# Optimization experiments

Measured on AMD Instinct MI355X. Metric: run time of the kernel, lower is better.

## Reference

```python
import jax, jax.numpy as jnp
import numpy as np

N = 50000      # nodes
E = 800000     # edges (before self-loops)
F_IN = 128     # input features
HID = 64       # hidden width
CLS = 40       # classes
NEG_SLOPE = 0.2  # PyG GATConv default
EPS = 1e-16


def setup_inputs() -> dict:
    key = jax.random.key(0)
    ks = jax.random.split(key, 16)

    def lin(k, fi, fo):
        return jax.random.normal(k, (fi, fo), jnp.float32) / np.float32(np.sqrt(fi))

    def att(k, f):
        return jax.random.normal(k, (f,), jnp.float32) / np.float32(np.sqrt(f))

    return {
        "x": jax.random.normal(ks[0], (N, F_IN), jnp.float32),
        "edge_index": jax.random.randint(ks[1], (2, E), 0, N, dtype=jnp.int64),
        "W1": lin(ks[2], F_IN, HID), "a_src1": att(ks[3], HID), "a_dst1": att(ks[4], HID), "b1": jnp.zeros((HID,), jnp.float32),
        "W2": lin(ks[5], HID, HID),  "a_src2": att(ks[6], HID), "a_dst2": att(ks[7], HID), "b2": jnp.zeros((HID,), jnp.float32),
        "W3": lin(ks[8], HID, CLS),  "a_src3": att(ks[9], CLS), "a_dst3": att(ks[10], CLS), "b3": jnp.zeros((CLS,), jnp.float32),
    }


def gat_layer(x, src, dst, W, a_src, a_dst, b, n):
    # Single-head GATConv (PyG semantics, heads=1, add_self_loops already applied).
    h = x @ W                                  # [n, out]
    s_src = h @ a_src                          # [n]
    s_dst = h @ a_dst                          # [n]
    e = jax.nn.leaky_relu(s_src[src] + s_dst[dst], NEG_SLOPE)  # [E']
    # softmax over incoming edges of each destination node
    m = jax.ops.segment_max(e, dst, num_segments=n)            # [n]
    e = jnp.exp(e - m[dst])
    denom = jax.ops.segment_sum(e, dst, num_segments=n)        # [n]
    alpha = e / (denom[dst] + EPS)                             # [E']
    out = jax.ops.segment_sum(h[src] * alpha[:, None], dst, num_segments=n)
    return out + b


def reference(x, edge_index, W1, a_src1, a_dst1, b1, W2, a_src2, a_dst2, b2, W3, a_src3, a_dst3, b3):
    n = x.shape[0]
    loop = jnp.arange(n, dtype=edge_index.dtype)
    src = jnp.concatenate([edge_index[0], loop])   # add self-loops (GATConv default)
    dst = jnp.concatenate([edge_index[1], loop])

    h = gat_layer(x, src, dst, W1, a_src1, a_dst1, b1, n)
    h = jax.nn.gelu(h, approximate=False)          # torch F.gelu default = exact erf
    h = gat_layer(h, src, dst, W2, a_src2, a_dst2, b2, n)
    h = jax.nn.gelu(h, approximate=False)
    out = gat_layer(h, src, dst, W3, a_src3, a_dst3, b3, n)
    return out
```

## Files before the change

kernel.cpp:

```cpp
#include <hip/hip_runtime.h>
#include <hip/hip_bf16.h>
#include <math.h>


#define PAD_CAP 64
#define SCAT_BLOCKS 128

__device__ __forceinline__ int detect64(const int* __restrict__ ei) {
  int any = 0;
#pragma unroll
  for (int i = 1; i < 64; i += 2) any |= ei[i];
  return any == 0;
}

__device__ __forceinline__ void load_edge(const int* __restrict__ ei, int E,
                                          int e, int is64, int n, int& s,
                                          int& d) {
  if (is64) {
    s = ei[2 * e];
    d = ei[2 * (E + e)];
  } else {
    s = ei[e];
    d = ei[E + e];
  }
  s = min(max(s, 0), n - 1);
  d = min(max(d, 0), n - 1);
}

template <int FROW>
__device__ __forceinline__ void gather8(const unsigned short* __restrict__ hu,
                                        int s0, float w0, int deg, int q,
                                        bool act, float& ax, float& ay,
                                        float& az, float& aw_) {
  int ss[8];
  float ww[8];
  uint2 hv[8];
#pragma unroll
  for (int j = 0; j < 8; ++j) {
    ss[j] = __shfl(s0, 4 * j + q);
    ww[j] = __shfl(w0, 4 * j + q);
  }
#pragma unroll
  for (int j = 0; j < 8; ++j) {
    hv[j].x = 0u;
    hv[j].y = 0u;
    if (act) hv[j] = *(const uint2*)(hu + (size_t)ss[j] * FROW);
  }
#pragma unroll
  for (int j = 0; j < 8; ++j) {
    ax = fmaf(ww[j], __uint_as_float(hv[j].x << 16), ax);
    ay = fmaf(ww[j], __uint_as_float(hv[j].x & 0xffff0000u), ay);
    az = fmaf(ww[j], __uint_as_float(hv[j].y << 16), az);
    aw_ = fmaf(ww[j], __uint_as_float(hv[j].y & 0xffff0000u), aw_);
  }
  const int dg4 = (deg + 3) >> 2;
  for (int g = 8; g < dg4; ++g) {
    const int ss1 = __shfl(s0, 4 * g + q);
    const float ww1 = __shfl(w0, 4 * g + q);
    uint2 hv1;
    hv1.x = 0u;
    hv1.y = 0u;
    if (act) hv1 = *(const uint2*)(hu + (size_t)ss1 * FROW);
    ax = fmaf(ww1, __uint_as_float(hv1.x << 16), ax);
    ay = fmaf(ww1, __uint_as_float(hv1.x & 0xffff0000u), ay);
    az = fmaf(ww1, __uint_as_float(hv1.y << 16), az);
    aw_ = fmaf(ww1, __uint_as_float(hv1.y & 0xffff0000u), aw_);
  }
}


template <int F_IN, int F_OUT, bool SCATTER>
__global__ __launch_bounds__(256) void gemm_att(
    const float* __restrict__ x, const float* __restrict__ W,
    const float* __restrict__ a_src, const float* __restrict__ a_dst,
    __hip_bfloat16* __restrict__ h, float* __restrict__ s_src,
    float* __restrict__ s_dst, int n, const int* __restrict__ ei, int E,
    int* __restrict__ deg, unsigned short* __restrict__ col) {
  if constexpr (SCATTER) {
    if (blockIdx.x < SCAT_BLOCKS) {
      const int is64 = detect64(ei);
      const int total = E + n;
      const int stride = SCAT_BLOCKS * 256;
      int e = blockIdx.x * 256 + threadIdx.x;
      while (e < total) {
        int sv[8], dv[8], va[8], pos[8];
#pragma unroll
        for (int j = 0; j < 8; ++j) {
          const int ee = e + j * stride;
          va[j] = (ee < total);
          int s = 0, d = 0;
          if (va[j]) {
            if (ee < E) load_edge(ei, E, ee, is64, n, s, d);
            else { s = ee - E; d = ee - E; }
          }
          sv[j] = s;
          dv[j] = d;
        }
#pragma unroll
        for (int j = 0; j < 8; ++j)
          pos[j] = va[j] ? atomicAdd(deg + dv[j], 1) : PAD_CAP;
#pragma unroll
        for (int j = 0; j < 8; ++j)
          if (va[j] && pos[j] < PAD_CAP)
            col[((size_t)dv[j] << 6) + pos[j]] = (unsigned short)sv[j];
        e += 8 * stride;
      }
      return;
    }
  }

  constexpr int TF = F_OUT / 4;
  __shared__ float Xt[F_IN * 65];
  __shared__ float red[2][4][64];
  const int wave = threadIdx.x >> 6, lane = threadIdx.x & 63;
  const int bid = SCATTER ? (int)blockIdx.x - SCAT_BLOCKS : (int)blockIdx.x;
  const int nb0 = bid * 64;
  const int node = nb0 + lane;

  {
    constexpr int Q = F_IN / 4;
    for (int i = threadIdx.x; i < 64 * Q; i += 256) {
      const int nd = i / Q, k4 = i % Q;
      float4 v = {0.f, 0.f, 0.f, 0.f};
      if (nb0 + nd < n)
        v = *(const float4*)(x + (size_t)(nb0 + nd) * F_IN + 4 * k4);
      Xt[(4 * k4 + 0) * 65 + nd] = v.x;
      Xt[(4 * k4 + 1) * 65 + nd] = v.y;
      Xt[(4 * k4 + 2) * 65 + nd] = v.z;
      Xt[(4 * k4 + 3) * 65 + nd] = v.w;
    }
  }
  __syncthreads();

  const int f0 = __builtin_amdgcn_readfirstlane(wave * TF);
  float acc[TF];
#pragma unroll
  for (int ff = 0; ff < TF; ++ff) acc[ff] = 0.f;

#pragma unroll 4
  for (int k = 0; k < F_IN; ++k) {
    const float xk = Xt[k * 65 + lane];
#pragma unroll
    for (int ff = 0; ff < TF; ++ff)
      acc[ff] = fmaf(xk, W[k * F_OUT + f0 + ff], acc[ff]);
  }

  float pa = 0.f, pb = 0.f;
#pragma unroll
  for (int ff = 0; ff < TF; ++ff) {
    pa = fmaf(acc[ff], a_src[f0 + ff], pa);
    pb = fmaf(acc[ff], a_dst[f0 + ff], pb);
  }
  if (node < n) {
#pragma unroll
    for (int ff = 0; ff < TF; ++ff)
      h[(size_t)node * F_OUT + f0 + ff] = __float2bfloat16(acc[ff]);
  }
  red[0][wave][lane] = pa;
  red[1][wave][lane] = pb;
  __syncthreads();
  if (wave == 0 && node < n) {
    s_src[node] = red[0][0][lane] + red[0][1][lane] + red[0][2][lane] +
                  red[0][3][lane];
    s_dst[node] = red[1][0][lane] + red[1][1][lane] + red[1][2][lane] +
                  red[1][3][lane];
  }
}

template <int F_OUT>
__global__ __launch_bounds__(1024, 4) void aggr_gemm(
    const unsigned short* __restrict__ col, const int* __restrict__ deg_arr,
    const float* __restrict__ ssrc, const float* __restrict__ sdst,
    const __hip_bfloat16* __restrict__ h_in, const float* __restrict__ bias_in,
    const float* __restrict__ W, const float* __restrict__ a_src,
    const float* __restrict__ a_dst, __hip_bfloat16* __restrict__ h_out,
    float* __restrict__ ssrc_out, float* __restrict__ sdst_out, int n) {
  constexpr int F_IN = 64;
  constexpr int NW = F_OUT / 4;
  __shared__ float Xt[F_IN * 65];
  __shared__ float red[2][16][64];
  const int wave = threadIdx.x >> 6, lane = threadIdx.x & 63;
  const int q = lane >> 4, t4 = lane & 15;
  const int nb0 = blockIdx.x * 64;

  float4 bv = make_float4(0.f, 0.f, 0.f, 0.f);
  if (lane < 16) bv = *(const float4*)(bias_in + 4 * lane);

  const unsigned short* __restrict__ hu = (const unsigned short*)h_in + 4 * t4;

  int degv[4], s0v[4];
  float sdv[4], svalv[4];
#pragma unroll
  for (int r = 0; r < 4; ++r) {
    const int d = nb0 + 4 * wave + r;
    const bool ok = d < n;
    degv[r] = ok ? min(deg_arr[d], PAD_CAP) : 0;
    sdv[r] = ok ? sdst[d] : 0.f;
    s0v[r] = 0;
    if (lane < degv[r]) s0v[r] = col[((size_t)d << 6) + lane];
  }
#pragma unroll
  for (int r = 0; r < 4; ++r) {
    svalv[r] = 0.f;
    if (lane < degv[r]) svalv[r] = ssrc[s0v[r]];
  }
  float w0v[4], invv[4];
#pragma unroll
  for (int r = 0; r < 4; ++r) {
    float w = 0.f;
    if (lane < degv[r]) {
      float t = svalv[r] + sdv[r];
      t = t > 0.f ? t : 0.2f * t;
      w = __expf(t);
    }
    w0v[r] = w;
  }
#pragma unroll
  for (int r = 0; r < 4; ++r) {
    float den = w0v[r];
#pragma unroll
    for (int off = 32; off > 0; off >>= 1) den += __shfl_xor(den, off);
    invv[r] = 1.f / (den + 1e-16f);
  }

  uint2 hv[4][8];
#pragma unroll
  for (int r = 0; r < 4; ++r) {
#pragma unroll
    for (int j = 0; j < 8; ++j) {
      const int ss = __shfl(s0v[r], 4 * j + q);
      hv[r][j] = *(const uint2*)(hu + (size_t)ss * F_IN);
    }
  }

#pragma unroll
  for (int r = 0; r < 4; ++r) {
    const int dl = 4 * wave + r;
    const int d = nb0 + dl;
    float ax = 0.f, ay = 0.f, az = 0.f, aw_ = 0.f;
#pragma unroll
    for (int j = 0; j < 8; ++j) {
      const float ww = __shfl(w0v[r], 4 * j + q);
      ax = fmaf(ww, __uint_as_float(hv[r][j].x << 16), ax);
      ay = fmaf(ww, __uint_as_float(hv[r][j].x & 0xffff0000u), ay);
      az = fmaf(ww, __uint_as_float(hv[r][j].y << 16), az);
      aw_ = fmaf(ww, __uint_as_float(hv[r][j].y & 0xffff0000u), aw_);
    }
    const int dg4 = (degv[r] + 3) >> 2;
    for (int g = 8; g < dg4; ++g) {
      const int ss1 = __shfl(s0v[r], 4 * g + q);
      const float ww1 = __shfl(w0v[r], 4 * g + q);
      const uint2 hv1 = *(const uint2*)(hu + (size_t)ss1 * F_IN);
      ax = fmaf(ww1, __uint_as_float(hv1.x << 16), ax);
      ay = fmaf(ww1, __uint_as_float(hv1.x & 0xffff0000u), ay);
      az = fmaf(ww1, __uint_as_float(hv1.y << 16), az);
      aw_ = fmaf(ww1, __uint_as_float(hv1.y & 0xffff0000u), aw_);
    }
#pragma unroll
    for (int off = 32; off >= 16; off >>= 1) {
      ax += __shfl_xor(ax, off);
      ay += __shfl_xor(ay, off);
      az += __shfl_xor(az, off);
      aw_ += __shfl_xor(aw_, off);
    }
    if (lane < 16) {
      float r0 = 0.f, r1 = 0.f, r2 = 0.f, r3 = 0.f;
      if (d < n) {
        r0 = ax * invv[r] + bv.x;
        r1 = ay * invv[r] + bv.y;
        r2 = az * invv[r] + bv.z;
        r3 = aw_ * invv[r] + bv.w;
        r0 = 0.5f * r0 * (1.f + erff(r0 * 0.70710678118654752f));
        r1 = 0.5f * r1 * (1.f + erff(r1 * 0.70710678118654752f));
        r2 = 0.5f * r2 * (1.f + erff(r2 * 0.70710678118654752f));
        r3 = 0.5f * r3 * (1.f + erff(r3 * 0.70710678118654752f));
      }
      Xt[(4 * lane + 0) * 65 + dl] = r0;
      Xt[(4 * lane + 1) * 65 + dl] = r1;
      Xt[(4 * lane + 2) * 65 + dl] = r2;
      Xt[(4 * lane + 3) * 65 + dl] = r3;
    }
  }
  __syncthreads();

  float pa = 0.f, pb = 0.f;
  const int node = nb0 + lane;
  if (wave < NW) {
    const int f0 = __builtin_amdgcn_readfirstlane(wave * 4);
    float acc[4] = {0.f, 0.f, 0.f, 0.f};
#pragma unroll 4
    for (int k = 0; k < F_IN; ++k) {
      const float xk = Xt[k * 65 + lane];
#pragma unroll
      for (int ff = 0; ff < 4; ++ff)
        acc[ff] = fmaf(xk, W[k * F_OUT + f0 + ff], acc[ff]);
    }
#pragma unroll
    for (int ff = 0; ff < 4; ++ff) {
      pa = fmaf(acc[ff], a_src[f0 + ff], pa);
      pb = fmaf(acc[ff], a_dst[f0 + ff], pb);
    }
    if (node < n) {
#pragma unroll
      for (int ff = 0; ff < 4; ++ff)
        h_out[(size_t)node * F_OUT + f0 + ff] = __float2bfloat16(acc[ff]);
    }
  }
  red[0][wave][lane] = pa;
  red[1][wave][lane] = pb;
  __syncthreads();
  if (wave == 0 && node < n) {
    float sa = 0.f, sb = 0.f;
#pragma unroll
    for (int w = 0; w < NW; ++w) {
      sa += red[0][w][lane];
      sb += red[1][w][lane];
    }
    ssrc_out[node] = sa;
    sdst_out[node] = sb;
  }
}

template <int F_OUT>
__global__ __launch_bounds__(256, 8) void attn_aggr(
    const unsigned short* __restrict__ col, const int* __restrict__ deg_arr,
    const float* __restrict__ ssrc, const float* __restrict__ sdst,
    const __hip_bfloat16* __restrict__ h, const float* __restrict__ bias,
    float* __restrict__ out, int n) {
  constexpr int NF4 = (F_OUT + 3) / 4;
  const int wave = threadIdx.x >> 6, lane = threadIdx.x & 63;
  const int q = lane >> 4, t4 = lane & 15;
  const int d = blockIdx.x * 4 + wave;
  if (d >= n) return;
  const bool act = (t4 < NF4);
  const unsigned short* __restrict__ hu = (const unsigned short*)h + 4 * t4;

  float4 bv = make_float4(0.f, 0.f, 0.f, 0.f);
  if (lane < NF4) bv = *(const float4*)(bias + 4 * lane);

  const int deg = min(deg_arr[d], PAD_CAP);
  const float sd = sdst[d];
  int s0 = 0;
  float w0 = 0.f;
  if (lane < deg) s0 = col[((size_t)d << 6) + lane];
  float sval = 0.f;
  if (lane < deg) sval = ssrc[s0];
  if (lane < deg) {
    float t = sval + sd;
    t = t > 0.f ? t : 0.2f * t;
    w0 = __expf(t);
  }
  float den = w0;
#pragma unroll
  for (int off = 32; off > 0; off >>= 1) den += __shfl_xor(den, off);
  const float inv = 1.f / (den + 1e-16f);

  float ax = 0.f, ay = 0.f, az = 0.f, aw_ = 0.f;
  gather8<F_OUT>(hu, s0, w0, deg, q, act, ax, ay, az, aw_);
#pragma unroll
  for (int off = 32; off >= 16; off >>= 1) {
    ax += __shfl_xor(ax, off);
    ay += __shfl_xor(ay, off);
    az += __shfl_xor(az, off);
    aw_ += __shfl_xor(aw_, off);
  }

  if (lane < NF4) {
    float r0 = ax * inv + bv.x;
    float r1 = ay * inv + bv.y;
    float r2 = az * inv + bv.z;
    float r3 = aw_ * inv + bv.w;
    *(float4*)(out + (size_t)d * F_OUT + 4 * lane) =
        make_float4(r0, r1, r2, r3);
  }
}

extern "C" void kernel_launch(void* const* d_in, const int* in_sizes, int n_in,
                              void* d_out, int out_size, void* d_ws,
                              size_t ws_size, hipStream_t stream) {
  const float* x = (const float*)d_in[0];
  const int* ei = (const int*)d_in[1];
  const float* W1 = (const float*)d_in[2];
  const float* as1 = (const float*)d_in[3];
  const float* ad1 = (const float*)d_in[4];
  const float* b1 = (const float*)d_in[5];
  const float* W2 = (const float*)d_in[6];
  const float* as2 = (const float*)d_in[7];
  const float* ad2 = (const float*)d_in[8];
  const float* b2 = (const float*)d_in[9];
  const float* W3 = (const float*)d_in[10];
  const float* as3 = (const float*)d_in[11];
  const float* ad3 = (const float*)d_in[12];
  const float* b3 = (const float*)d_in[13];

  const int n = in_sizes[0] / 128;
  const int E = in_sizes[1] / 2;

  const size_t need = ((size_t)n * (32 + 32 + 1 + 1 + 1 + 1 + 1 + 32)) * 4 + 256;
  if (ws_size < need) return;

  __hip_bfloat16* hbA = (__hip_bfloat16*)d_ws;
  __hip_bfloat16* hbB = hbA + (size_t)n * 64;
  float* ssrcA = (float*)d_ws + (size_t)n * 64;
  float* sdstA = ssrcA + n;
  float* ssrcB = sdstA + n;
  float* sdstB = ssrcB + n;
  int* deg = (int*)(sdstB + n);
  unsigned short* col = (unsigned short*)(deg + n);

  const int gemm_blocks = (n + 63) / 64;
  const int aggr3_blocks = (n + 3) / 4;

  hipMemsetAsync(deg, 0, (size_t)n * 4, stream);
  gemm_att<128, 64, true><<<gemm_blocks + SCAT_BLOCKS, 256, 0, stream>>>(
      x, W1, as1, ad1, hbA, ssrcA, sdstA, n, ei, E, deg, col);

  aggr_gemm<64><<<gemm_blocks, 1024, 0, stream>>>(
      col, deg, ssrcA, sdstA, hbA, b1, W2, as2, ad2, hbB, ssrcB, sdstB, n);

  aggr_gemm<40><<<gemm_blocks, 1024, 0, stream>>>(
      col, deg, ssrcB, sdstB, hbB, b2, W3, as3, ad3, hbA, ssrcA, sdstA, n);

  attn_aggr<40><<<aggr3_blocks, 256, 0, stream>>>(
      col, deg, ssrcA, sdstA, hbA, b3, (float*)d_out, n);
}
```

Baseline: 281.4 us.

## Shard edge scatter by destination range and cut aggr_gemm register pressure

The CSR-building scatter now splits its blocks into 8 shards, each owning a contiguous destination-node range. Each block scans a strided subset of all edges and keeps only those whose destination falls in its shard, so the atomics and column writes from one block land in a narrower memory region. In aggr_gemm, the 4x8 gathered-row prefetch array is replaced by a per-row 8-wide prefetch and launch_bounds rises to 8 waves per EU, trading gather memory-level parallelism for occupancy. Because every shard now reads every edge, edge-index read traffic goes up about 8x. The gather8 helper is also inlined by hand.

```diff
diff --git a/kernel.cpp b/kernel.cpp
--- a/kernel.cpp
+++ b/kernel.cpp
@@ -25,47 +25,6 @@
   }
   s = min(max(s, 0), n - 1);
   d = min(max(d, 0), n - 1);
-}
-
-template <int FROW>
-__device__ __forceinline__ void gather8(const unsigned short* __restrict__ hu,
-                                        int s0, float w0, int deg, int q,
-                                        bool act, float& ax, float& ay,
-                                        float& az, float& aw_) {
-  int ss[8];
-  float ww[8];
-  uint2 hv[8];
-#pragma unroll
-  for (int j = 0; j < 8; ++j) {
-    ss[j] = __shfl(s0, 4 * j + q);
-    ww[j] = __shfl(w0, 4 * j + q);
-  }
-#pragma unroll
-  for (int j = 0; j < 8; ++j) {
-    hv[j].x = 0u;
-    hv[j].y = 0u;
-    if (act) hv[j] = *(const uint2*)(hu + (size_t)ss[j] * FROW);
-  }
-#pragma unroll
-  for (int j = 0; j < 8; ++j) {
-    ax = fmaf(ww[j], __uint_as_float(hv[j].x << 16), ax);
-    ay = fmaf(ww[j], __uint_as_float(hv[j].x & 0xffff0000u), ay);
-    az = fmaf(ww[j], __uint_as_float(hv[j].y << 16), az);
-    aw_ = fmaf(ww[j], __uint_as_float(hv[j].y & 0xffff0000u), aw_);
-  }
-  const int dg4 = (deg + 3) >> 2;
-  for (int g = 8; g < dg4; ++g) {
-    const int ss1 = __shfl(s0, 4 * g + q);
-    const float ww1 = __shfl(w0, 4 * g + q);
-    uint2 hv1;
-    hv1.x = 0u;
-    hv1.y = 0u;
-    if (act) hv1 = *(const uint2*)(hu + (size_t)ss1 * FROW);
-    ax = fmaf(ww1, __uint_as_float(hv1.x << 16), ax);
-    ay = fmaf(ww1, __uint_as_float(hv1.x & 0xffff0000u), ay);
-    az = fmaf(ww1, __uint_as_float(hv1.y << 16), az);
-    aw_ = fmaf(ww1, __uint_as_float(hv1.y & 0xffff0000u), aw_);
-  }
 }
 
 
@@ -80,19 +39,25 @@
     if (blockIdx.x < SCAT_BLOCKS) {
       const int is64 = detect64(ei);
       const int total = E + n;
-      const int stride = SCAT_BLOCKS * 256;
-      int e = blockIdx.x * 256 + threadIdx.x;
+      const int shard = blockIdx.x & 7;
+      const int sub = blockIdx.x >> 3;
+      const int lo = (int)(((long long)shard * n) >> 3);
+      const int hi = (int)(((long long)(shard + 1) * n) >> 3);
+      const int stride16 = 16 * 256;
+      int e = sub * 256 + threadIdx.x;
       while (e < total) {
         int sv[8], dv[8], va[8], pos[8];
 #pragma unroll
         for (int j = 0; j < 8; ++j) {
-          const int ee = e + j * stride;
-          va[j] = (ee < total);
+          const int ee = e + j * stride16;
           int s = 0, d = 0;
-          if (va[j]) {
+          int v = (ee < total);
+          if (v) {
             if (ee < E) load_edge(ei, E, ee, is64, n, s, d);
             else { s = ee - E; d = ee - E; }
+            v = (d >= lo) && (d < hi);
           }
+          va[j] = v;
           sv[j] = s;
           dv[j] = d;
         }
@@ -103,7 +68,7 @@
         for (int j = 0; j < 8; ++j)
           if (va[j] && pos[j] < PAD_CAP)
             col[((size_t)dv[j] << 6) + pos[j]] = (unsigned short)sv[j];
-        e += 8 * stride;
+        e += 8 * stride16;
       }
       return;
     }
@@ -168,7 +133,7 @@
 }
 
 template <int F_OUT>
-__global__ __launch_bounds__(1024, 4) void aggr_gemm(
+__global__ __launch_bounds__(1024, 8) void aggr_gemm(
     const unsigned short* __restrict__ col, const int* __restrict__ deg_arr,
     const float* __restrict__ ssrc, const float* __restrict__ sdst,
     const __hip_bfloat16* __restrict__ h_in, const float* __restrict__ bias_in,
@@ -223,38 +188,40 @@
     invv[r] = 1.f / (den + 1e-16f);
   }
 
-  uint2 hv[4][8];
-#pragma unroll
-  for (int r = 0; r < 4; ++r) {
-#pragma unroll
-    for (int j = 0; j < 8; ++j) {
-      const int ss = __shfl(s0v[r], 4 * j + q);
-      hv[r][j] = *(const uint2*)(hu + (size_t)ss * F_IN);
-    }
-  }
-
 #pragma unroll
   for (int r = 0; r < 4; ++r) {
     const int dl = 4 * wave + r;
     const int d = nb0 + dl;
     float ax = 0.f, ay = 0.f, az = 0.f, aw_ = 0.f;
-#pragma unroll
-    for (int j = 0; j < 8; ++j) {
-      const float ww = __shfl(w0v[r], 4 * j + q);
-      ax = fmaf(ww, __uint_as_float(hv[r][j].x << 16), ax);
-      ay = fmaf(ww, __uint_as_float(hv[r][j].x & 0xffff0000u), ay);
-      az = fmaf(ww, __uint_as_float(hv[r][j].y << 16), az);
-      aw_ = fmaf(ww, __uint_as_float(hv[r][j].y & 0xffff0000u), aw_);
-    }
-    const int dg4 = (degv[r] + 3) >> 2;
-    for (int g = 8; g < dg4; ++g) {
-      const int ss1 = __shfl(s0v[r], 4 * g + q);
-      const float ww1 = __shfl(w0v[r], 4 * g + q);
-      const uint2 hv1 = *(const uint2*)(hu + (size_t)ss1 * F_IN);
-      ax = fmaf(ww1, __uint_as_float(hv1.x << 16), ax);
-      ay = fmaf(ww1, __uint_as_float(hv1.x & 0xffff0000u), ay);
-      az = fmaf(ww1, __uint_as_float(hv1.y << 16), az);
-      aw_ = fmaf(ww1, __uint_as_float(hv1.y & 0xffff0000u), aw_);
+    {
+      int ss[8];
+      float ww[8];
+      uint2 hv[8];
+#pragma unroll
+      for (int j = 0; j < 8; ++j) {
+        ss[j] = __shfl(s0v[r], 4 * j + q);
+        ww[j] = __shfl(w0v[r], 4 * j + q);
+      }
+#pragma unroll
+      for (int j = 0; j < 8; ++j)
+        hv[j] = *(const uint2*)(hu + (size_t)ss[j] * F_IN);
+#pragma unroll
+      for (int j = 0; j < 8; ++j) {
+        ax = fmaf(ww[j], __uint_as_float(hv[j].x << 16), ax);
+        ay = fmaf(ww[j], __uint_as_float(hv[j].x & 0xffff0000u), ay);
+        az = fmaf(ww[j], __uint_as_float(hv[j].y << 16), az);
+        aw_ = fmaf(ww[j], __uint_as_float(hv[j].y & 0xffff0000u), aw_);
+      }
+      const int dg4 = (degv[r] + 3) >> 2;
+      for (int g = 8; g < dg4; ++g) {
+        const int ss1 = __shfl(s0v[r], 4 * g + q);
+        const float ww1 = __shfl(w0v[r], 4 * g + q);
+        const uint2 hv1 = *(const uint2*)(hu + (size_t)ss1 * F_IN);
+        ax = fmaf(ww1, __uint_as_float(hv1.x << 16), ax);
+        ay = fmaf(ww1, __uint_as_float(hv1.x & 0xffff0000u), ay);
+        az = fmaf(ww1, __uint_as_float(hv1.y << 16), az);
+        aw_ = fmaf(ww1, __uint_as_float(hv1.y & 0xffff0000u), aw_);
+      }
     }
 #pragma unroll
     for (int off = 32; off >= 16; off >>= 1) {
@@ -356,7 +323,42 @@
   const float inv = 1.f / (den + 1e-16f);
 
   float ax = 0.f, ay = 0.f, az = 0.f, aw_ = 0.f;
-  gather8<F_OUT>(hu, s0, w0, deg, q, act, ax, ay, az, aw_);
+  {
+    int ss[8];
+    float ww[8];
+    uint2 hv[8];
+#pragma unroll
+    for (int j = 0; j < 8; ++j) {
+      ss[j] = __shfl(s0, 4 * j + q);
+      ww[j] = __shfl(w0, 4 * j + q);
+    }
+#pragma unroll
+    for (int j = 0; j < 8; ++j) {
+      hv[j].x = 0u;
+      hv[j].y = 0u;
+      if (act) hv[j] = *(const uint2*)(hu + (size_t)ss[j] * F_OUT);
+    }
+#pragma unroll
+    for (int j = 0; j < 8; ++j) {
+      ax = fmaf(ww[j], __uint_as_float(hv[j].x << 16), ax);
+      ay = fmaf(ww[j], __uint_as_float(hv[j].x & 0xffff0000u), ay);
+      az = fmaf(ww[j], __uint_as_float(hv[j].y << 16), az);
+      aw_ = fmaf(ww[j], __uint_as_float(hv[j].y & 0xffff0000u), aw_);
+    }
+    const int dg4 = (deg + 3) >> 2;
+    for (int g = 8; g < dg4; ++g) {
+      const int ss1 = __shfl(s0, 4 * g + q);
+      const float ww1 = __shfl(w0, 4 * g + q);
+      uint2 hv1;
+      hv1.x = 0u;
+      hv1.y = 0u;
+      if (act) hv1 = *(const uint2*)(hu + (size_t)ss1 * F_OUT);
+      ax = fmaf(ww1, __uint_as_float(hv1.x << 16), ax);
+      ay = fmaf(ww1, __uint_as_float(hv1.x & 0xffff0000u), ay);
+      az = fmaf(ww1, __uint_as_float(hv1.y << 16), az);
+      aw_ = fmaf(ww1, __uint_as_float(hv1.y & 0xffff0000u), aw_);
+    }
+  }
 #pragma unroll
   for (int off = 32; off >= 16; off >>= 1) {
     ax += __shfl_xor(ax, off);
```

After: 314.9 us. 1.12x slower.
